# Kernel tuning notes

Hardware: AMD Instinct MI355X
Metric: run time of the kernel (lower is better)

## Reference

```python
import jax, jax.numpy as jnp
import numpy as np

N = 50000      # nodes
E = 800000     # edges
IN = 128       # in_size
H = 128        # hid_size
OUT = 40       # out_size
L = 3          # num_hid_layers
K = 32         # maxk


def _xavier(key, shape):
    fan_in, fan_out = shape[0], shape[1]
    limit = np.sqrt(6.0 / (fan_in + fan_out))
    return jax.random.uniform(key, shape, jnp.float32, -limit, limit)


def setup_inputs() -> dict:
    key = jax.random.key(0)
    ks = jax.random.split(key, 16)
    x = jax.random.normal(ks[0], (N, IN), jnp.float32)
    src = jax.random.randint(ks[1], (E,), 0, N, jnp.int32)
    dst = jax.random.randint(ks[2], (E,), 0, N, jnp.int32)
    # weights stored as [in, out] so forward is x @ W + b (math-equivalent to torch Linear)
    W_in = _xavier(ks[3], (IN, H)); b_in = jnp.zeros((H,), jnp.float32)
    W_lin = jnp.stack([_xavier(jax.random.fold_in(ks[4], i), (H, H)) for i in range(L)])
    b_lin = jnp.zeros((L, H), jnp.float32)
    W1 = jnp.stack([_xavier(jax.random.fold_in(ks[5], i), (H, H)) for i in range(L)])
    b1 = jnp.zeros((L, H), jnp.float32)
    W2 = jnp.stack([_xavier(jax.random.fold_in(ks[6], i), (H, H)) for i in range(L)])
    b2 = jnp.zeros((L, H), jnp.float32)
    eps = jnp.zeros((L,), jnp.float32)  # learnable eps, init 0
    W_out = _xavier(ks[7], (H, OUT)); b_out = jnp.zeros((OUT,), jnp.float32)
    return {"x": x, "src": src, "dst": dst, "W_in": W_in, "b_in": b_in,
            "W_lin": W_lin, "b_lin": b_lin, "W1": W1, "b1": b1,
            "W2": W2, "b2": b2, "eps": eps, "W_out": W_out, "b_out": b_out}


def _maxk(h, k):
    # keep top-k entries per row, zero the rest (threshold form; ties negligible for random floats)
    thr = jax.lax.top_k(h, k)[0][:, -1:]  # [N, 1] kth-largest value
    return jnp.where(h >= thr, h, 0.0)


def reference(x, src, dst, W_in, b_in, W_lin, b_lin, W1, b1, W2, b2, eps, W_out, b_out):
    h = jax.nn.relu(x @ W_in + b_in)  # [N, H]
    for i in range(L):
        h = h @ W_lin[i] + b_lin[i]
        # GIN conv with MaxK sparsified messages (dropout p=0 / eval mode)
        hs = _maxk(h, K)                                             # [N, H] top-K sparse
        neigh = jax.ops.segment_sum(hs[src], dst, num_segments=N)    # copy_u + sum
        o = (1.0 + eps[i]) * h + neigh
        h = jax.nn.relu(o @ W1[i] + b1[i]) @ W2[i] + b2[i]
    return h @ W_out + b_out  # [N, OUT]
```

## Files before the change

### kernel.cpp

```cpp
#include <hip/hip_runtime.h>

typedef __bf16 bf16x8 __attribute__((ext_vector_type(8)));
typedef float f32x4 __attribute__((ext_vector_type(4)));

__device__ inline unsigned short f2b(float f) {
  unsigned int u = __float_as_uint(f);
  u += 0x7fffu + ((u >> 16) & 1u);
  return (unsigned short)(u >> 16);
}
__device__ inline float b2f(unsigned short u) {
  return __uint_as_float(((unsigned int)u) << 16);
}

__device__ inline int swz(int r, int c) { return r * 128 + (c ^ ((r & 7) << 3)); }

__device__ inline bf16x8 ldfrag(const unsigned short* p) {
  uint4 v = *(const uint4*)p;
  bf16x8 r;
  __builtin_memcpy(&r, &v, 16);
  return r;
}

__global__ __launch_bounds__(256) void prep_wt(
    const float* __restrict__ W_in, const float* __restrict__ W_lin,
    const float* __restrict__ W1, const float* __restrict__ W2,
    const float* __restrict__ W_out, unsigned short* __restrict__ Wh,
    unsigned short* __restrict__ Wl)
{
  int slot = blockIdx.y;
  int e = blockIdx.x * 256 + threadIdx.x;
  int n = e >> 7, k = e & 127;
  const float* srcp; int N;
  if (slot == 0)      { srcp = W_in;                   N = 128; }
  else if (slot < 4)  { srcp = W_lin + (slot-1)*16384; N = 128; }
  else if (slot < 7)  { srcp = W1   + (slot-4)*16384;  N = 128; }
  else if (slot < 10) { srcp = W2   + (slot-7)*16384;  N = 128; }
  else                { srcp = W_out;                  N = 40;  }
  float v = (n < N) ? srcp[k * N + n] : 0.f;
  unsigned short hi = f2b(v);
  float lo = v - b2f(hi);
  Wh[slot * 16384 + e] = hi;
  Wl[slot * 16384 + e] = f2b(lo);
}

template<int TPB, int WM, int WN, int MF, int NF, bool RELU>
__global__ __launch_bounds__(TPB) void gemm_k(
    const float* __restrict__ Ap, const unsigned short* __restrict__ Wh,
    const unsigned short* __restrict__ Wl, const float* __restrict__ bias,
    float* __restrict__ Cp, int M, int Ncols)
{
  constexpr int BM = WM * MF * 16;
  static_assert(WM * WN * 64 == TPB, "wave count");
  static_assert(BM * 128 % (TPB * 4) == 0, "");
  __shared__ __align__(16) unsigned short ldsAh[BM * 128];
  __shared__ __align__(16) unsigned short ldsAl[BM * 128];

  const int tid = threadIdx.x;
  const int row0 = blockIdx.x * BM;

  constexpr int AIT = BM * 128 / (TPB * 4);
#pragma unroll
  for (int it = 0; it < AIT; ++it) {
    int flat = it * (TPB * 4) + tid * 4;
    int r = flat >> 7, c = flat & 127;
    int gr = row0 + r;
    float4 v = make_float4(0.f, 0.f, 0.f, 0.f);
    if (gr < M) v = *(const float4*)(Ap + (size_t)gr * 128 + c);
    ushort4 h4, l4;
    h4.x = f2b(v.x); l4.x = f2b(v.x - b2f(h4.x));
    h4.y = f2b(v.y); l4.y = f2b(v.y - b2f(h4.y));
    h4.z = f2b(v.z); l4.z = f2b(v.z - b2f(h4.z));
    h4.w = f2b(v.w); l4.w = f2b(v.w - b2f(h4.w));
    *(ushort4*)&ldsAh[swz(r, c)] = h4;
    *(ushort4*)&ldsAl[swz(r, c)] = l4;
  }
  __syncthreads();

  const int wid = tid >> 6, lane = tid & 63;
  const int wm = wid / WN, wn = wid % WN;
  const int l15 = lane & 15, lk = lane >> 4;

  f32x4 acc[MF][NF];
#pragma unroll
  for (int mi = 0; mi < MF; ++mi)
#pragma unroll
    for (int ni = 0; ni < NF; ++ni)
      acc[mi][ni] = (f32x4){0.f, 0.f, 0.f, 0.f};

  const unsigned short* wbh = Wh + (size_t)(wn * NF * 16 + l15) * 128;
  const unsigned short* wbl = Wl + (size_t)(wn * NF * 16 + l15) * 128;

#pragma unroll
  for (int kk = 0; kk < 4; ++kk) {
    const int kc = kk * 32 + lk * 8;
    bf16x8 ah[MF], al[MF];
#pragma unroll
    for (int mi = 0; mi < MF; ++mi) {
      int rr = wm * MF * 16 + mi * 16 + l15;
      ah[mi] = ldfrag(&ldsAh[swz(rr, kc)]);
      al[mi] = ldfrag(&ldsAl[swz(rr, kc)]);
    }
    bf16x8 bh[NF], bl[NF];
#pragma unroll
    for (int ni = 0; ni < NF; ++ni) {
      bh[ni] = ldfrag(wbh + ni * 16 * 128 + kc);
      bl[ni] = ldfrag(wbl + ni * 16 * 128 + kc);
    }
#pragma unroll
    for (int mi = 0; mi < MF; ++mi)
#pragma unroll
      for (int ni = 0; ni < NF; ++ni) {
        acc[mi][ni] = __builtin_amdgcn_mfma_f32_16x16x32_bf16(ah[mi], bl[ni], acc[mi][ni], 0, 0, 0);
        acc[mi][ni] = __builtin_amdgcn_mfma_f32_16x16x32_bf16(al[mi], bh[ni], acc[mi][ni], 0, 0, 0);
        acc[mi][ni] = __builtin_amdgcn_mfma_f32_16x16x32_bf16(ah[mi], bh[ni], acc[mi][ni], 0, 0, 0);
      }
  }

#pragma unroll
  for (int ni = 0; ni < NF; ++ni) {
    int col = wn * NF * 16 + ni * 16 + l15;
    if (col >= Ncols) continue;
    float bc = bias[col];
#pragma unroll
    for (int mi = 0; mi < MF; ++mi) {
      int rbase = row0 + wm * MF * 16 + mi * 16 + lk * 4;
#pragma unroll
      for (int j = 0; j < 4; ++j) {
        int r = rbase + j;
        if (r >= M) continue;
        float v = acc[mi][ni][j] + bc;
        if (RELU) v = fmaxf(v, 0.f);
        Cp[(size_t)r * Ncols + col] = v;
      }
    }
  }
}

__global__ __launch_bounds__(512) void fusedgemm_k(
    const float* __restrict__ h2, const float* __restrict__ neigh,
    const float* __restrict__ epsp,
    const unsigned short* __restrict__ Wh1, const unsigned short* __restrict__ Wl1,
    const float* __restrict__ b1,
    const unsigned short* __restrict__ Wh2, const unsigned short* __restrict__ Wl2,
    const float* __restrict__ b2, float* __restrict__ Hout, int M)
{
  constexpr int WM = 2, WN = 4, MF = 2, NF = 2;
  constexpr int BM = WM * MF * 16;
  __shared__ __align__(16) unsigned short ldsAh[BM * 128];
  __shared__ __align__(16) unsigned short ldsAl[BM * 128];

  const int tid = threadIdx.x;
  const int row0 = blockIdx.x * BM;
  const float epsf = 1.0f + epsp[0];

#pragma unroll
  for (int it = 0; it < BM * 128 / 2048; ++it) {
    int flat = it * 2048 + tid * 4;
    int r = flat >> 7, c = flat & 127;
    int gr = row0 + r;
    float4 v = make_float4(0.f, 0.f, 0.f, 0.f);
    if (gr < M) {
      v = *(const float4*)(h2 + (size_t)gr * 128 + c);
      float4 ng = *(const float4*)(neigh + (size_t)gr * 128 + c);
      v = make_float4(fmaf(epsf, v.x, ng.x), fmaf(epsf, v.y, ng.y),
                      fmaf(epsf, v.z, ng.z), fmaf(epsf, v.w, ng.w));
    }
    ushort4 h4, l4;
    h4.x = f2b(v.x); l4.x = f2b(v.x - b2f(h4.x));
    h4.y = f2b(v.y); l4.y = f2b(v.y - b2f(h4.y));
    h4.z = f2b(v.z); l4.z = f2b(v.z - b2f(h4.z));
    h4.w = f2b(v.w); l4.w = f2b(v.w - b2f(h4.w));
    *(ushort4*)&ldsAh[swz(r, c)] = h4;
    *(ushort4*)&ldsAl[swz(r, c)] = l4;
  }
  __syncthreads();

  const int wid = tid >> 6, lane = tid & 63;
  const int wm = wid / WN, wn = wid % WN;
  const int l15 = lane & 15, lk = lane >> 4;

  f32x4 acc[MF][NF];
#pragma unroll
  for (int mi = 0; mi < MF; ++mi)
#pragma unroll
    for (int ni = 0; ni < NF; ++ni)
      acc[mi][ni] = (f32x4){0.f, 0.f, 0.f, 0.f};

  {
    const unsigned short* wbh = Wh1 + (size_t)(wn * NF * 16 + l15) * 128;
    const unsigned short* wbl = Wl1 + (size_t)(wn * NF * 16 + l15) * 128;
#pragma unroll
    for (int kk = 0; kk < 4; ++kk) {
      const int kc = kk * 32 + lk * 8;
      bf16x8 ah[MF], al[MF];
#pragma unroll
      for (int mi = 0; mi < MF; ++mi) {
        int rr = wm * MF * 16 + mi * 16 + l15;
        ah[mi] = ldfrag(&ldsAh[swz(rr, kc)]);
        al[mi] = ldfrag(&ldsAl[swz(rr, kc)]);
      }
      bf16x8 bh[NF], bl[NF];
#pragma unroll
      for (int ni = 0; ni < NF; ++ni) {
        bh[ni] = ldfrag(wbh + ni * 16 * 128 + kc);
        bl[ni] = ldfrag(wbl + ni * 16 * 128 + kc);
      }
#pragma unroll
      for (int mi = 0; mi < MF; ++mi)
#pragma unroll
        for (int ni = 0; ni < NF; ++ni) {
          acc[mi][ni] = __builtin_amdgcn_mfma_f32_16x16x32_bf16(ah[mi], bl[ni], acc[mi][ni], 0, 0, 0);
          acc[mi][ni] = __builtin_amdgcn_mfma_f32_16x16x32_bf16(al[mi], bh[ni], acc[mi][ni], 0, 0, 0);
          acc[mi][ni] = __builtin_amdgcn_mfma_f32_16x16x32_bf16(ah[mi], bh[ni], acc[mi][ni], 0, 0, 0);
        }
    }
  }
  __syncthreads();

#pragma unroll
  for (int ni = 0; ni < NF; ++ni) {
    int c = wn * NF * 16 + ni * 16 + l15;
    float bc = b1[c];
#pragma unroll
    for (int mi = 0; mi < MF; ++mi) {
#pragma unroll
      for (int j = 0; j < 4; ++j) {
        int r = wm * MF * 16 + mi * 16 + lk * 4 + j;
        float v = fmaxf(acc[mi][ni][j] + bc, 0.f);
        unsigned short hi = f2b(v);
        ldsAh[swz(r, c)] = hi;
        ldsAl[swz(r, c)] = f2b(v - b2f(hi));
        acc[mi][ni][j] = 0.f;
      }
    }
  }
  __syncthreads();

  {
    const unsigned short* wbh = Wh2 + (size_t)(wn * NF * 16 + l15) * 128;
    const unsigned short* wbl = Wl2 + (size_t)(wn * NF * 16 + l15) * 128;
#pragma unroll
    for (int kk = 0; kk < 4; ++kk) {
      const int kc = kk * 32 + lk * 8;
      bf16x8 ah[MF], al[MF];
#pragma unroll
      for (int mi = 0; mi < MF; ++mi) {
        int rr = wm * MF * 16 + mi * 16 + l15;
        ah[mi] = ldfrag(&ldsAh[swz(rr, kc)]);
        al[mi] = ldfrag(&ldsAl[swz(rr, kc)]);
      }
      bf16x8 bh[NF], bl[NF];
#pragma unroll
      for (int ni = 0; ni < NF; ++ni) {
        bh[ni] = ldfrag(wbh + ni * 16 * 128 + kc);
        bl[ni] = ldfrag(wbl + ni * 16 * 128 + kc);
      }
#pragma unroll
      for (int mi = 0; mi < MF; ++mi)
#pragma unroll
        for (int ni = 0; ni < NF; ++ni) {
          acc[mi][ni] = __builtin_amdgcn_mfma_f32_16x16x32_bf16(ah[mi], bl[ni], acc[mi][ni], 0, 0, 0);
          acc[mi][ni] = __builtin_amdgcn_mfma_f32_16x16x32_bf16(al[mi], bh[ni], acc[mi][ni], 0, 0, 0);
          acc[mi][ni] = __builtin_amdgcn_mfma_f32_16x16x32_bf16(ah[mi], bh[ni], acc[mi][ni], 0, 0, 0);
        }
    }
  }

#pragma unroll
  for (int ni = 0; ni < NF; ++ni) {
    int col = wn * NF * 16 + ni * 16 + l15;
    float bc = b2[col];
#pragma unroll
    for (int mi = 0; mi < MF; ++mi) {
#pragma unroll
      for (int j = 0; j < 4; ++j) {
        int r = row0 + wm * MF * 16 + mi * 16 + lk * 4 + j;
        if (r >= M) continue;
        Hout[(size_t)r * 128 + col] = acc[mi][ni][j] + bc;
      }
    }
  }
}

__global__ __launch_bounds__(256) void maxk_k(const float* __restrict__ h,
                                              unsigned int* __restrict__ hs, int M)
{
  int row = blockIdx.x * 4 + (threadIdx.x >> 6);
  if (row >= M) return;
  int lane = threadIdx.x & 63;
  float2 pr = *(const float2*)(h + (size_t)row * 128 + lane * 2);
  auto key = [](float f) -> unsigned int {
    unsigned int b = __float_as_uint(f);
    return (b & 0x80000000u) ? ~b : (b | 0x80000000u);
  };
  unsigned int k0 = key(pr.x), k1 = key(pr.y);
  unsigned int thr = 0;
#pragma unroll
  for (int b = 31; b >= 0; --b) {
    unsigned int t = thr | (1u << b);
    int c = __popcll(__ballot(k0 >= t)) + __popcll(__ballot(k1 >= t));
    if (c >= 32) thr = t;
  }
  unsigned long long g0 = __ballot(k0 > thr), g1 = __ballot(k1 > thr);
  unsigned long long e0 = __ballot(k0 == thr), e1 = __ballot(k1 == thr);
  int cgt = __popcll(g0) + __popcll(g1);
  unsigned long long mlt = (1ull << lane) - 1ull;
  unsigned long long mle = mlt | (1ull << lane);
  bool keep0 = (k0 > thr) ||
               ((k0 == thr) && (cgt + __popcll(e0 & mlt) + __popcll(e1 & mlt)) < 32);
  bool keep1 = (k1 > thr) ||
               ((k1 == thr) && (cgt + __popcll(e0 & mle) + __popcll(e1 & mlt)) < 32);
  unsigned int w0 = keep0 ? (unsigned int)f2b(pr.x) : 0u;
  unsigned int w1 = keep1 ? (unsigned int)f2b(pr.y) : 0u;
  hs[(size_t)row * 64 + lane] = w0 | (w1 << 16);
}

__global__ __launch_bounds__(256) void hist_k(const int* __restrict__ dst,
                                              int* __restrict__ cnt, int E)
{
  int e = blockIdx.x * 256 + threadIdx.x;
  if (e < E) atomicAdd(&cnt[dst[e]], 1);
}

__global__ __launch_bounds__(256) void bsum_k(const int* __restrict__ cnt,
                                              int* __restrict__ bsum, int M)
{
  __shared__ int s[256];
  int i = blockIdx.x * 256 + threadIdx.x;
  int t = threadIdx.x;
  s[t] = (i < M) ? cnt[i] : 0;
  __syncthreads();
  for (int st = 128; st > 0; st >>= 1) {
    if (t < st) s[t] += s[t + st];
    __syncthreads();
  }
  if (t == 0) bsum[blockIdx.x] = s[0];
}

__global__ __launch_bounds__(1024) void scanb_k(int* __restrict__ bsum, int NB)
{
  __shared__ int s[1024];
  int t = threadIdx.x;
  int v = (t < NB) ? bsum[t] : 0;
  s[t] = v;
  __syncthreads();
  for (int st = 1; st < 1024; st <<= 1) {
    int a = (t >= st) ? s[t - st] : 0;
    __syncthreads();
    s[t] += a;
    __syncthreads();
  }
  if (t < NB) bsum[t] = s[t] - v;
}

__global__ __launch_bounds__(256) void scano_k(const int* __restrict__ cnt,
                                               const int* __restrict__ bsum,
                                               int* __restrict__ offs,
                                               int* __restrict__ cur, int M, int E)
{
  __shared__ int s[256];
  int i = blockIdx.x * 256 + threadIdx.x;
  int t = threadIdx.x;
  int v = (i < M) ? cnt[i] : 0;
  s[t] = v;
  __syncthreads();
  for (int st = 1; st < 256; st <<= 1) {
    int a = (t >= st) ? s[t - st] : 0;
    __syncthreads();
    s[t] += a;
    __syncthreads();
  }
  int excl = s[t] - v + bsum[blockIdx.x];
  if (i < M) { offs[i] = excl; cur[i] = excl; }
  if (blockIdx.x == 0 && t == 0) offs[M] = E;
}

__global__ __launch_bounds__(256) void fill_k(const int* __restrict__ src,
                                              const int* __restrict__ dst,
                                              int* __restrict__ cur,
                                              unsigned short* __restrict__ eidx, int E)
{
  int e = blockIdx.x * 256 + threadIdx.x;
  if (e >= E) return;
  int d = dst[e];
  int p = atomicAdd(&cur[d], 1);
  eidx[p] = (unsigned short)src[e];
}

__global__ __launch_bounds__(256) void gather_k(
    const unsigned int* __restrict__ hs, const int* __restrict__ offs,
    const unsigned short* __restrict__ eidx, float* __restrict__ neigh, int M)
{
  const int w = threadIdx.x >> 6, lane = threadIdx.x & 63;
  const int d = blockIdx.x * 4 + w;
  if (d >= M) return;
  const int start = offs[d], end = offs[d + 1];
  float ax = 0.f, ay = 0.f;
  int i = start;
  for (; i + 4 <= end; i += 4) {
    int s0 = eidx[i], s1 = eidx[i + 1], s2 = eidx[i + 2], s3 = eidx[i + 3];
    unsigned int u0 = hs[(size_t)s0 * 64 + lane];
    unsigned int u1 = hs[(size_t)s1 * 64 + lane];
    unsigned int u2 = hs[(size_t)s2 * 64 + lane];
    unsigned int u3 = hs[(size_t)s3 * 64 + lane];
    ax += (b2f(u0 & 0xffffu) + b2f(u1 & 0xffffu)) +
          (b2f(u2 & 0xffffu) + b2f(u3 & 0xffffu));
    ay += (b2f(u0 >> 16) + b2f(u1 >> 16)) + (b2f(u2 >> 16) + b2f(u3 >> 16));
  }
  for (; i < end; ++i) {
    unsigned int u0 = hs[(size_t)eidx[i] * 64 + lane];
    ax += b2f(u0 & 0xffffu);
    ay += b2f(u0 >> 16);
  }
  float2 o;
  o.x = ax;
  o.y = ay;
  *(float2*)(neigh + (size_t)d * 128 + (size_t)lane * 2) = o;
}

extern "C" void kernel_launch(void* const* d_in, const int* in_sizes, int n_in,
                              void* d_out, int out_size, void* d_ws, size_t ws_size,
                              hipStream_t stream)
{
  const float* x     = (const float*)d_in[0];
  const int*   src   = (const int*)d_in[1];
  const int*   dst   = (const int*)d_in[2];
  const float* W_in  = (const float*)d_in[3];
  const float* b_in  = (const float*)d_in[4];
  const float* W_lin = (const float*)d_in[5];
  const float* b_lin = (const float*)d_in[6];
  const float* W1    = (const float*)d_in[7];
  const float* b1    = (const float*)d_in[8];
  const float* W2    = (const float*)d_in[9];
  const float* b2    = (const float*)d_in[10];
  const float* eps   = (const float*)d_in[11];
  const float* W_out = (const float*)d_in[12];
  const float* b_out = (const float*)d_in[13];

  const int M = in_sizes[0] / 128;
  const int E = in_sizes[1];

  const int NB = (M + 255) / 256;
  char* ws = (char*)d_ws;
  unsigned short* Wh = (unsigned short*)ws;
  size_t off = (size_t)11 * 16384 * 2;
  unsigned short* Wl = (unsigned short*)(ws + off); off += (size_t)11 * 16384 * 2;
  float* PA    = (float*)(ws + off); off += (size_t)M * 128 * 4;
  float* PB    = (float*)(ws + off); off += (size_t)M * 128 * 4;
  float* neigh = (float*)(ws + off); off += (size_t)M * 128 * 4;
  int* offs = (int*)(ws + off); off += (size_t)(M + 1) * 4;
  unsigned short* eidx = (unsigned short*)(ws + off); off += (size_t)E * 2;
  int* cnt  = (int*)(ws + off); off += (size_t)M * 4;
  int* cur  = (int*)(ws + off); off += (size_t)M * 4;
  int* bsum = (int*)(ws + off); off += (size_t)NB * 4;

  dim3 blk(256);
  dim3 blk512(512);
  prep_wt<<<dim3(64, 11), blk, 0, stream>>>(W_in, W_lin, W1, W2, W_out, Wh, Wl);

  (void)hipMemsetAsync(cnt, 0, (size_t)M * 4, stream);
  hist_k<<<(E + 255) / 256, blk, 0, stream>>>(dst, cnt, E);
  bsum_k<<<NB, blk, 0, stream>>>(cnt, bsum, M);
  scanb_k<<<1, 1024, 0, stream>>>(bsum, NB);
  scano_k<<<NB, blk, 0, stream>>>(cnt, bsum, offs, cur, M, E);
  fill_k<<<(E + 255) / 256, blk, 0, stream>>>(src, dst, cur, eidx, E);

  const int gm64 = (M + 63) / 64;

  float* hbuf = PA;
  float* h2buf = PB;
  gemm_k<512,2,4,2,2,true><<<gm64, blk512, 0, stream>>>(
      x, Wh, Wl, b_in, hbuf, M, 128);

  for (int i = 0; i < 3; ++i) {
    const size_t wlin_off = (size_t)(1 + i) * 16384;
    const size_t w1_off   = (size_t)(4 + i) * 16384;
    const size_t w2_off   = (size_t)(7 + i) * 16384;
    gemm_k<512,2,4,2,2,false><<<gm64, blk512, 0, stream>>>(
        hbuf, Wh + wlin_off, Wl + wlin_off, b_lin + i * 128, h2buf, M, 128);
    unsigned int* hs = (unsigned int*)hbuf;
    maxk_k<<<(M + 3) / 4, blk, 0, stream>>>(h2buf, hs, M);
    gather_k<<<(M + 3) / 4, blk, 0, stream>>>(hs, offs, eidx, neigh, M);
    fusedgemm_k<<<gm64, blk512, 0, stream>>>(
        h2buf, neigh, eps + i, Wh + w1_off, Wl + w1_off, b1 + i * 128,
        Wh + w2_off, Wl + w2_off, b2 + i * 128, hbuf, M);
  }

  const size_t wo_off = (size_t)10 * 16384;
  gemm_k<256,4,1,1,3,false><<<gm64, blk, 0, stream>>>(
      hbuf, Wh + wo_off, Wl + wo_off, b_out, (float*)d_out, M, 40);
}
```

Before: 604.1 us.

## Fuse MaxK top-k sparsification into the linear GEMM epilogue via LDS

Removes the standalone maxk kernel. The W_lin GEMM stages its output tile in shared memory and runs the ballot-based top-k threshold search per row, one wave per row. It writes the packed bf16 sparse rows straight into the input buffer at a 128-word row stride, so each block overwrites only its own already-consumed input rows. This saves a full re-read of h2 and one launch per layer, at the cost of extra barriers and LDS reuse in the GEMM and a sparser stride for the gather. The gather loop is also unrolled to 8 edges for more memory-level parallelism.

```diff
diff --git a/kernel.cpp b/kernel.cpp
--- a/kernel.cpp
+++ b/kernel.cpp
@@ -43,17 +43,18 @@
   Wl[slot * 16384 + e] = f2b(lo);
 }
 
-template<int TPB, int WM, int WN, int MF, int NF, bool RELU>
+template<int TPB, int WM, int WN, int MF, int NF, bool RELU, bool MAXK>
 __global__ __launch_bounds__(TPB) void gemm_k(
     const float* __restrict__ Ap, const unsigned short* __restrict__ Wh,
     const unsigned short* __restrict__ Wl, const float* __restrict__ bias,
-    float* __restrict__ Cp, int M, int Ncols)
+    float* __restrict__ Cp, int M, int Ncols, unsigned int* __restrict__ hs)
 {
   constexpr int BM = WM * MF * 16;
   static_assert(WM * WN * 64 == TPB, "wave count");
   static_assert(BM * 128 % (TPB * 4) == 0, "");
-  __shared__ __align__(16) unsigned short ldsAh[BM * 128];
-  __shared__ __align__(16) unsigned short ldsAl[BM * 128];
+  __shared__ __align__(16) unsigned short ldsBuf[BM * 128 * 2];
+  unsigned short* ldsAh = ldsBuf;
+  unsigned short* ldsAl = ldsBuf + BM * 128;
 
   const int tid = threadIdx.x;
   const int row0 = blockIdx.x * BM;
@@ -116,6 +117,9 @@
       }
   }
 
+  if constexpr (MAXK) __syncthreads();
+  float* tile = (float*)ldsBuf;
+
 #pragma unroll
   for (int ni = 0; ni < NF; ++ni) {
     int col = wn * NF * 16 + ni * 16 + l15;
@@ -123,15 +127,52 @@
     float bc = bias[col];
 #pragma unroll
     for (int mi = 0; mi < MF; ++mi) {
-      int rbase = row0 + wm * MF * 16 + mi * 16 + lk * 4;
+      int lr = wm * MF * 16 + mi * 16 + lk * 4;
 #pragma unroll
       for (int j = 0; j < 4; ++j) {
-        int r = rbase + j;
-        if (r >= M) continue;
+        int r = row0 + lr + j;
         float v = acc[mi][ni][j] + bc;
         if (RELU) v = fmaxf(v, 0.f);
-        Cp[(size_t)r * Ncols + col] = v;
-      }
+        if constexpr (MAXK) tile[(lr + j) * 128 + col] = v;
+        if (r < M) Cp[(size_t)r * Ncols + col] = v;
+      }
+    }
+  }
+
+  if constexpr (MAXK) {
+    __syncthreads();
+    constexpr int NW = TPB / 64;
+    constexpr int ROWS = BM / NW;
+#pragma unroll
+    for (int rr = 0; rr < ROWS; ++rr) {
+      int lrow = wid * ROWS + rr;
+      int grow = row0 + lrow;
+      if (grow >= M) break;
+      float2 pr = *(const float2*)&tile[lrow * 128 + lane * 2];
+      auto key = [](float f) -> unsigned int {
+        unsigned int b = __float_as_uint(f);
+        return (b & 0x80000000u) ? ~b : (b | 0x80000000u);
+      };
+      unsigned int k0 = key(pr.x), k1 = key(pr.y);
+      unsigned int thr = 0;
+#pragma unroll
+      for (int b = 31; b >= 0; --b) {
+        unsigned int t = thr | (1u << b);
+        int c = __popcll(__ballot(k0 >= t)) + __popcll(__ballot(k1 >= t));
+        if (c >= 32) thr = t;
+      }
+      unsigned long long g0 = __ballot(k0 > thr), g1 = __ballot(k1 > thr);
+      unsigned long long e0 = __ballot(k0 == thr), e1 = __ballot(k1 == thr);
+      int cgt = __popcll(g0) + __popcll(g1);
+      unsigned long long mlt = (1ull << lane) - 1ull;
+      unsigned long long mle = mlt | (1ull << lane);
+      bool keep0 = (k0 > thr) ||
+                   ((k0 == thr) && (cgt + __popcll(e0 & mlt) + __popcll(e1 & mlt)) < 32);
+      bool keep1 = (k1 > thr) ||
+                   ((k1 == thr) && (cgt + __popcll(e0 & mle) + __popcll(e1 & mlt)) < 32);
+      unsigned int w0 = keep0 ? (unsigned int)f2b(pr.x) : 0u;
+      unsigned int w1 = keep1 ? (unsigned int)f2b(pr.y) : 0u;
+      hs[(size_t)grow * 128 + lane] = w0 | (w1 << 16);
     }
   }
 }
@@ -282,39 +323,6 @@
   }
 }
 
-__global__ __launch_bounds__(256) void maxk_k(const float* __restrict__ h,
-                                              unsigned int* __restrict__ hs, int M)
-{
-  int row = blockIdx.x * 4 + (threadIdx.x >> 6);
-  if (row >= M) return;
-  int lane = threadIdx.x & 63;
-  float2 pr = *(const float2*)(h + (size_t)row * 128 + lane * 2);
-  auto key = [](float f) -> unsigned int {
-    unsigned int b = __float_as_uint(f);
-    return (b & 0x80000000u) ? ~b : (b | 0x80000000u);
-  };
-  unsigned int k0 = key(pr.x), k1 = key(pr.y);
-  unsigned int thr = 0;
-#pragma unroll
-  for (int b = 31; b >= 0; --b) {
-    unsigned int t = thr | (1u << b);
-    int c = __popcll(__ballot(k0 >= t)) + __popcll(__ballot(k1 >= t));
-    if (c >= 32) thr = t;
-  }
-  unsigned long long g0 = __ballot(k0 > thr), g1 = __ballot(k1 > thr);
-  unsigned long long e0 = __ballot(k0 == thr), e1 = __ballot(k1 == thr);
-  int cgt = __popcll(g0) + __popcll(g1);
-  unsigned long long mlt = (1ull << lane) - 1ull;
-  unsigned long long mle = mlt | (1ull << lane);
-  bool keep0 = (k0 > thr) ||
-               ((k0 == thr) && (cgt + __popcll(e0 & mlt) + __popcll(e1 & mlt)) < 32);
-  bool keep1 = (k1 > thr) ||
-               ((k1 == thr) && (cgt + __popcll(e0 & mle) + __popcll(e1 & mlt)) < 32);
-  unsigned int w0 = keep0 ? (unsigned int)f2b(pr.x) : 0u;
-  unsigned int w1 = keep1 ? (unsigned int)f2b(pr.y) : 0u;
-  hs[(size_t)row * 64 + lane] = w0 | (w1 << 16);
-}
-
 __global__ __launch_bounds__(256) void hist_k(const int* __restrict__ dst,
                                               int* __restrict__ cnt, int E)
 {
@@ -397,18 +405,30 @@
   const int start = offs[d], end = offs[d + 1];
   float ax = 0.f, ay = 0.f;
   int i = start;
+  for (; i + 8 <= end; i += 8) {
+    unsigned int u0 = hs[(size_t)eidx[i]     * 128 + lane];
+    unsigned int u1 = hs[(size_t)eidx[i + 1] * 128 + lane];
+    unsigned int u2 = hs[(size_t)eidx[i + 2] * 128 + lane];
+    unsigned int u3 = hs[(size_t)eidx[i + 3] * 128 + lane];
+    unsigned int u4 = hs[(size_t)eidx[i + 4] * 128 + lane];
+    unsigned int u5 = hs[(size_t)eidx[i + 5] * 128 + lane];
+    unsigned int u6 = hs[(size_t)eidx[i + 6] * 128 + lane];
+    unsigned int u7 = hs[(size_t)eidx[i + 7] * 128 + lane];
+    ax += ((b2f(u0 & 0xffffu) + b2f(u1 & 0xffffu)) + (b2f(u2 & 0xffffu) + b2f(u3 & 0xffffu))) +
+          ((b2f(u4 & 0xffffu) + b2f(u5 & 0xffffu)) + (b2f(u6 & 0xffffu) + b2f(u7 & 0xffffu)));
+    ay += ((b2f(u0 >> 16) + b2f(u1 >> 16)) + (b2f(u2 >> 16) + b2f(u3 >> 16))) +
+          ((b2f(u4 >> 16) + b2f(u5 >> 16)) + (b2f(u6 >> 16) + b2f(u7 >> 16)));
+  }
   for (; i + 4 <= end; i += 4) {
-    int s0 = eidx[i], s1 = eidx[i + 1], s2 = eidx[i + 2], s3 = eidx[i + 3];
-    unsigned int u0 = hs[(size_t)s0 * 64 + lane];
-    unsigned int u1 = hs[(size_t)s1 * 64 + lane];
-    unsigned int u2 = hs[(size_t)s2 * 64 + lane];
-    unsigned int u3 = hs[(size_t)s3 * 64 + lane];
-    ax += (b2f(u0 & 0xffffu) + b2f(u1 & 0xffffu)) +
-          (b2f(u2 & 0xffffu) + b2f(u3 & 0xffffu));
+    unsigned int u0 = hs[(size_t)eidx[i]     * 128 + lane];
+    unsigned int u1 = hs[(size_t)eidx[i + 1] * 128 + lane];
+    unsigned int u2 = hs[(size_t)eidx[i + 2] * 128 + lane];
+    unsigned int u3 = hs[(size_t)eidx[i + 3] * 128 + lane];
+    ax += (b2f(u0 & 0xffffu) + b2f(u1 & 0xffffu)) + (b2f(u2 & 0xffffu) + b2f(u3 & 0xffffu));
     ay += (b2f(u0 >> 16) + b2f(u1 >> 16)) + (b2f(u2 >> 16) + b2f(u3 >> 16));
   }
   for (; i < end; ++i) {
-    unsigned int u0 = hs[(size_t)eidx[i] * 64 + lane];
+    unsigned int u0 = hs[(size_t)eidx[i] * 128 + lane];
     ax += b2f(u0 & 0xffffu);
     ay += b2f(u0 >> 16);
   }
@@ -469,17 +489,16 @@
 
   float* hbuf = PA;
   float* h2buf = PB;
-  gemm_k<512,2,4,2,2,true><<<gm64, blk512, 0, stream>>>(
-      x, Wh, Wl, b_in, hbuf, M, 128);
+  gemm_k<512,2,4,2,2,true,false><<<gm64, blk512, 0, stream>>>(
+      x, Wh, Wl, b_in, hbuf, M, 128, nullptr);
 
   for (int i = 0; i < 3; ++i) {
     const size_t wlin_off = (size_t)(1 + i) * 16384;
     const size_t w1_off   = (size_t)(4 + i) * 16384;
     const size_t w2_off   = (size_t)(7 + i) * 16384;
-    gemm_k<512,2,4,2,2,false><<<gm64, blk512, 0, stream>>>(
-        hbuf, Wh + wlin_off, Wl + wlin_off, b_lin + i * 128, h2buf, M, 128);
     unsigned int* hs = (unsigned int*)hbuf;
-    maxk_k<<<(M + 3) / 4, blk, 0, stream>>>(h2buf, hs, M);
+    gemm_k<512,2,4,2,2,false,true><<<gm64, blk512, 0, stream>>>(
+        hbuf, Wh + wlin_off, Wl + wlin_off, b_lin + i * 128, h2buf, M, 128, hs);
     gather_k<<<(M + 3) / 4, blk, 0, stream>>>(hs, offs, eidx, neigh, M);
     fusedgemm_k<<<gm64, blk512, 0, stream>>>(
         h2buf, neigh, eps + i, Wh + w1_off, Wl + w1_off, b1 + i * 128,
@@ -487,6 +506,6 @@
   }
 
   const size_t wo_off = (size_t)10 * 16384;
-  gemm_k<256,4,1,1,3,false><<<gm64, blk, 0, stream>>>(
-      hbuf, Wh + wo_off, Wl + wo_off, b_out, (float*)d_out, M, 40);
-}
+  gemm_k<256,4,1,1,3,false,false><<<gm64, blk, 0, stream>>>(
+      hbuf, Wh + wo_off, Wl + wo_off, b_out, (float*)d_out, M, 40, nullptr);
+}
```

New measurement: 590.2 us. 2.3% less time.
